# Kernel optimization log

Measured on AMD Instinct MI355X. Metric: run time of the kernel, lower is better.

Reference implementation:

```python
import jax, jax.numpy as jnp
import numpy as np

DIM = 768
NUM_HEADS = 12
HEAD_DIM = DIM // NUM_HEADS
SCALE = HEAD_DIM ** -0.5


def setup_inputs() -> dict:
    key = jax.random.key(0)
    k1, k2, k3, k4 = jax.random.split(key, 4)
    B, N, C = 4, 2048, DIM
    x = jax.random.normal(k1, (B, N, C), dtype=jnp.float32)
    # nn.Linear(dim, 3*dim, bias=False): weight shape (3C, C), y = x @ W^T
    w_qkv = jax.random.normal(k2, (3 * C, C), dtype=jnp.float32) * (C ** -0.5)
    # nn.Linear(dim, dim) with default bias=True
    w_proj = jax.random.normal(k3, (C, C), dtype=jnp.float32) * (C ** -0.5)
    b_proj = jax.random.normal(k4, (C,), dtype=jnp.float32) * 0.02
    return {"x": x, "w_qkv": w_qkv, "w_proj": w_proj, "b_proj": b_proj}


def reference(x, w_qkv, w_proj, b_proj):
    B, N, C = x.shape
    H, D = NUM_HEADS, HEAD_DIM
    qkv = jnp.einsum('bnc,oc->bno', x, w_qkv)  # (B, N, 3C)
    qkv = qkv.reshape(B, N, 3, H, D).transpose(2, 0, 3, 1, 4)  # (3, B, H, N, D)
    q, k, v = qkv[0], qkv[1], qkv[2]
    attn = jnp.einsum('bhnd,bhmd->bhnm', q, k) * jnp.float32(SCALE)  # (B,H,N,N)
    attn = jax.nn.softmax(attn, axis=-1)
    out = jnp.einsum('bhnm,bhmd->bhnd', attn, v)  # (B,H,N,D)
    out = out.transpose(0, 2, 1, 3).reshape(B, N, C)
    out = jnp.einsum('bnc,oc->bno', out, w_proj) + b_proj
    return out
```

## Files before the change

kernel.cpp:

```cpp
#include <hip/hip_runtime.h>
#include <math.h>

#define B_ 4
#define N_ 2048
#define C_ 768
#define H_ 12
#define D_ 64
#define QKSCALE_ 0.18033688011112042f

typedef unsigned short u16;
typedef unsigned int u32;
typedef short s16x8 __attribute__((ext_vector_type(8)));
typedef float f32x4 __attribute__((ext_vector_type(4)));
typedef u32 u32x2 __attribute__((ext_vector_type(2)));

__device__ __forceinline__ u16 f2bf(float f) {
    union { float f; u32 u; } v; v.f = f;
    u32 r = (v.u + 0x7fffu + ((v.u >> 16) & 1u)) >> 16;
    return (u16)r;
}

__device__ __forceinline__ u32 pkbf(float a, float b) {
    union { float f; u32 u; } ua, ub; ua.f = a; ub.f = b;
    u32 ra = ua.u + 0x7fffu + ((ua.u >> 16) & 1u);
    u32 rb = ub.u + 0x7fffu + ((ub.u >> 16) & 1u);
    return __builtin_amdgcn_perm(rb, ra, 0x07060302u);
}

__device__ __forceinline__ void gl_lds16(const u16* g, u16* l) {
    __builtin_amdgcn_global_load_lds(
        (__attribute__((address_space(1))) void*)g,
        (__attribute__((address_space(3))) void*)l, 16, 0, 0);
}

#define NX4_  (B_ * N_ * C_ / 4)
#define NWQ4_ (3 * C_ * C_ / 4)
#define NWP4_ (C_ * C_ / 4)
__global__ __launch_bounds__(256) void cvt_all(const float4* __restrict__ x,
                                               const float4* __restrict__ wq,
                                               const float4* __restrict__ wp,
                                               ushort4* __restrict__ xb,
                                               ushort4* __restrict__ wqb,
                                               ushort4* __restrict__ wpb)
{
    const int tot = NX4_ + NWQ4_ + NWP4_;
    int i = blockIdx.x * blockDim.x + threadIdx.x;
    const int stride = gridDim.x * blockDim.x;
    for (; i < tot; i += stride) {
        const float4* s; ushort4* d; int j;
        if (i < NX4_)              { s = x;  d = xb;  j = i; }
        else if (i < NX4_ + NWQ4_) { s = wq; d = wqb; j = i - NX4_; }
        else                       { s = wp; d = wpb; j = i - NX4_ - NWQ4_; }
        float4 v = s[j];
        ushort4 o;
        o.x = f2bf(v.x); o.y = f2bf(v.y); o.z = f2bf(v.z); o.w = f2bf(v.w);
        d[j] = o;
    }
}

template<int BM, int WPEU, bool OUT_BF16, bool BIAS, bool QSCALE>
__global__ __launch_bounds__(256, WPEU) void gemm_mfma(const u16* __restrict__ A,
                                                       const u16* __restrict__ Bm,
                                                       const float* __restrict__ bias,
                                                       void* __restrict__ Cout,
                                                       int M, int N, int K)
{
    constexpr int MF = BM / 32;
    constexpr int ACALLS = BM / 64;
    constexpr int ASZ = BM * 32, BSZ = 128 * 32;
    __shared__ __align__(16) u16 As[2 * ASZ];
    __shared__ __align__(16) u16 Bs[2 * BSZ];
    const int tid  = threadIdx.x;
    const int wv   = tid >> 6;
    const int lane = tid & 63;
    const int lr   = lane & 15;
    const int lq   = lane >> 4;
    const int wm   = (wv >> 1) * (BM / 2);
    const int wn   = (wv & 1) * 64;
    const int row0 = blockIdx.y * BM, col0 = blockIdx.x * 128;

    f32x4 acc[MF][4];
    #pragma unroll
    for (int i = 0; i < MF; i++)
        #pragma unroll
        for (int j = 0; j < 4; j++) { f32x4 z = {0.f,0.f,0.f,0.f}; acc[i][j] = z; }

    const int srow   = lane >> 2;
    const int schunk = (((lane & 3) ^ ((lane >> 3) & 3)) * 8);

    const int arow_base = (BM / 4) * wv;
    const u16* gA0 = A + (size_t)(row0 + arow_base + srow) * K + schunk;
    const u16* gB0 = Bm + (size_t)(col0 + 32 * wv + srow) * K + schunk;
    const u16* gB1 = gB0 + (size_t)16 * K;
    const int aoff0 = arow_base * 32;
    const int boff0 = (32 * wv) * 32, boff1 = boff0 + 16 * 32;

    const int ppos = (lq ^ ((lr >> 1) & 3)) * 8;
    const int nIter = K / 32;

    #pragma unroll
    for (int c = 0; c < ACALLS; c++)
        gl_lds16(gA0 + (size_t)(16 * c) * K, As + aoff0 + c * 16 * 32);
    gl_lds16(gB0, Bs + boff0);
    gl_lds16(gB1, Bs + boff1);

    for (int t = 0; t < nIter; t++) {
        const int cur = t & 1;
        __syncthreads();
        if (t + 1 < nIter) {
            const int k1 = (t + 1) * 32;
            const int nb = cur ^ 1;
            #pragma unroll
            for (int c = 0; c < ACALLS; c++)
                gl_lds16(gA0 + (size_t)(16 * c) * K + k1,
                         As + nb * ASZ + aoff0 + c * 16 * 32);
            gl_lds16(gB0 + k1, Bs + nb * BSZ + boff0);
            gl_lds16(gB1 + k1, Bs + nb * BSZ + boff1);
        }
        const u16* __restrict__ Ac = As + cur * ASZ;
        const u16* __restrict__ Bc = Bs + cur * BSZ;
        s16x8 af[MF], bfr[4];
        #pragma unroll
        for (int i = 0; i < MF; i++)
            af[i] = *(const s16x8*)&Ac[(wm + 16*i + lr) * 32 + ppos];
        #pragma unroll
        for (int j = 0; j < 4; j++)
            bfr[j] = *(const s16x8*)&Bc[(wn + 16*j + lr) * 32 + ppos];
        #pragma unroll
        for (int i = 0; i < MF; i++)
            #pragma unroll
            for (int j = 0; j < 4; j++)
                acc[i][j] = __builtin_amdgcn_mfma_f32_16x16x32_bf16(af[i], bfr[j], acc[i][j], 0, 0, 0);
    }

    #pragma unroll
    for (int i = 0; i < MF; i++) {
        #pragma unroll
        for (int j = 0; j < 4; j++) {
            const int col = col0 + wn + 16*j + lr;
            float bv = BIAS ? bias[col] : 0.f;
            #pragma unroll
            for (int r = 0; r < 4; r++) {
                const int row = row0 + wm + 16*i + lq*4 + r;
                float v = acc[i][j][r] + bv;
                if (QSCALE && col < C_) v *= QKSCALE_;
                if (OUT_BF16) ((u16*)Cout)[(size_t)row * N + col] = f2bf(v);
                else          ((float*)Cout)[(size_t)row * N + col] = v;
            }
        }
    }
}

__global__ __launch_bounds__(256, 4) void attn_mfma(const u16* __restrict__ qkv,
                                                    u16* __restrict__ attout)
{
    __shared__ __align__(16) u16 Ks[64 * 64];
    __shared__ __align__(16) u16 Vt[64][72];
    __shared__ __align__(16) u16 Ps[128 * 64];

    const int tid  = threadIdx.x;
    const int wv   = tid >> 6;
    const int lane = tid & 63;
    const int lr   = lane & 15;
    const int lq   = lane >> 4;
    const int n0   = blockIdx.x * 128;
    const int bh   = blockIdx.y, b = bh / H_, h = bh % H_;
    const size_t rs = 3 * C_;

    const u16* Qg = qkv + ((size_t)b * N_ + n0) * rs + h * D_;
    const u16* Kg = qkv + ((size_t)b * N_) * rs + C_ + h * D_;
    const u16* Vg = Kg + C_;

    s16x8 qf[2][2];
    #pragma unroll
    for (int iq = 0; iq < 2; iq++)
        #pragma unroll
        for (int kk = 0; kk < 2; kk++)
            qf[iq][kk] = *(const s16x8*)(Qg + (size_t)(32*wv + 16*iq + lr) * rs + kk*32 + lq*8);

    f32x4 oacc[2][4];
    float li[2] = {0.f, 0.f};
    #pragma unroll
    for (int i = 0; i < 2; i++)
        #pragma unroll
        for (int j = 0; j < 4; j++) { f32x4 z = {0.f,0.f,0.f,0.f}; oacc[i][j] = z; }

    const int skey = tid >> 2;
    const int sc0  = (tid & 3) * 2;
    const int scA  = (sc0     ^ (skey & 7)) * 8;
    const int scB  = ((sc0+1) ^ (skey & 7)) * 8;
    const int vc = tid & 7, vp = tid >> 3;
    const int vkey0 = 2 * vp, vd0 = vc * 8;
    const int vcol0 = (vkey0 + 8 * vc) & 63;

    s16x8 kr0, kr1, vr0, vr1;
    {
        const u16* kp = Kg + (size_t)skey * rs + sc0 * 8;
        kr0 = *(const s16x8*)kp; kr1 = *(const s16x8*)(kp + 8);
        const u16* vp2 = Vg + (size_t)vkey0 * rs + vd0;
        vr0 = *(const s16x8*)vp2; vr1 = *(const s16x8*)(vp2 + rs);
    }

    for (int t = 0; t < N_ / 64; t++) {
        __syncthreads();
        *(s16x8*)&Ks[skey * 64 + scA] = kr0;
        *(s16x8*)&Ks[skey * 64 + scB] = kr1;
        #pragma unroll
        for (int u = 0; u < 8; u++) {
            u32 pk = (u32)(u16)vr0[u] | ((u32)(u16)vr1[u] << 16);
            *(u32*)&Vt[vd0 + u][vcol0] = pk;
        }
        __syncthreads();
        if (t + 1 < N_ / 64) {
            const u16* kp = Kg + (size_t)((t+1)*64 + skey) * rs + sc0 * 8;
            kr0 = *(const s16x8*)kp; kr1 = *(const s16x8*)(kp + 8);
            const u16* vp2 = Vg + (size_t)((t+1)*64 + vkey0) * rs + vd0;
            vr0 = *(const s16x8*)vp2; vr1 = *(const s16x8*)(vp2 + rs);
        }

        f32x4 st[4][2];
        #pragma unroll
        for (int jk = 0; jk < 4; jk++)
            #pragma unroll
            for (int iq = 0; iq < 2; iq++) { f32x4 z = {0.f,0.f,0.f,0.f}; st[jk][iq] = z; }
        #pragma unroll
        for (int kk = 0; kk < 2; kk++) {
            s16x8 kf[4];
            #pragma unroll
            for (int jk = 0; jk < 4; jk++)
                kf[jk] = *(const s16x8*)&Ks[(16*jk + lr) * 64 + ((4*kk + lq) ^ (lr & 7)) * 8];
            #pragma unroll
            for (int jk = 0; jk < 4; jk++) {
                st[jk][0] = __builtin_amdgcn_mfma_f32_16x16x32_bf16(kf[jk], qf[0][kk], st[jk][0], 0, 0, 0);
                st[jk][1] = __builtin_amdgcn_mfma_f32_16x16x32_bf16(kf[jk], qf[1][kk], st[jk][1], 0, 0, 0);
            }
        }

        #pragma unroll
        for (int jk = 0; jk < 4; jk++)
            #pragma unroll
            for (int iq = 0; iq < 2; iq++) {
                const float p0 = __builtin_amdgcn_exp2f(st[jk][iq][0]);
                const float p1 = __builtin_amdgcn_exp2f(st[jk][iq][1]);
                const float p2 = __builtin_amdgcn_exp2f(st[jk][iq][2]);
                const float p3 = __builtin_amdgcn_exp2f(st[jk][iq][3]);
                li[iq] += (p0 + p1) + (p2 + p3);
                u32x2 w;
                w.x = pkbf(p0, p1);
                w.y = pkbf(p2, p3);
                const int prow = 32*wv + 16*iq + lr;
                const int pch  = ((2*jk + (lq >> 1)) ^ (lr & 7)) * 8 + (lq & 1) * 4;
                *(u32x2*)&Ps[prow * 64 + pch] = w;
            }

        #pragma unroll
        for (int kk = 0; kk < 2; kk++) {
            s16x8 ap0 = *(const s16x8*)&Ps[(32*wv      + lr) * 64 + ((4*kk + lq) ^ (lr & 7)) * 8];
            s16x8 ap1 = *(const s16x8*)&Ps[(32*wv + 16 + lr) * 64 + ((4*kk + lq) ^ (lr & 7)) * 8];
            #pragma unroll
            for (int j2 = 0; j2 < 4; j2++) {
                const int pb = ((kk*4 + lq) + 2*j2 + (lr >> 3)) & 7;
                s16x8 bv = *(const s16x8*)&Vt[16*j2 + lr][pb * 8];
                oacc[0][j2] = __builtin_amdgcn_mfma_f32_16x16x32_bf16(ap0, bv, oacc[0][j2], 0, 0, 0);
                oacc[1][j2] = __builtin_amdgcn_mfma_f32_16x16x32_bf16(ap1, bv, oacc[1][j2], 0, 0, 0);
            }
        }
    }

    #pragma unroll
    for (int iq = 0; iq < 2; iq++) {
        li[iq] += __shfl_xor(li[iq], 16);
        li[iq] += __shfl_xor(li[iq], 32);
    }
    #pragma unroll
    for (int iq = 0; iq < 2; iq++) {
        #pragma unroll
        for (int r = 0; r < 4; r++) {
            const float inv = 1.f / __shfl(li[iq], 4*lq + r);
            const int row = n0 + 32*wv + 16*iq + 4*lq + r;
            #pragma unroll
            for (int j2 = 0; j2 < 4; j2++)
                attout[((size_t)(b * N_ + row)) * C_ + h * D_ + 16*j2 + lr] =
                    f2bf(oacc[iq][j2][r] * inv);
        }
    }
}

extern "C" void kernel_launch(void* const* d_in, const int* in_sizes, int n_in,
                              void* d_out, int out_size, void* d_ws, size_t ws_size,
                              hipStream_t stream) {
    const float* x      = (const float*)d_in[0];
    const float* w_qkv  = (const float*)d_in[1];
    const float* w_proj = (const float*)d_in[2];
    const float* b_proj = (const float*)d_in[3];
    float* out = (float*)d_out;

    const int NX   = B_ * N_ * C_;
    const int NWQ  = 3 * C_ * C_;
    const int NWP  = C_ * C_;
    const int NQKV = B_ * N_ * 3 * C_;

    u16* xb   = (u16*)d_ws;
    u16* wqb  = xb + NX;
    u16* wpb  = wqb + NWQ;
    u16* qkvb = wpb + NWP;
    u16* attb = qkvb + NQKV;

    dim3 blk(256);

    cvt_all<<<768, blk, 0, stream>>>((const float4*)x, (const float4*)w_qkv,
                                     (const float4*)w_proj,
                                     (ushort4*)xb, (ushort4*)wqb, (ushort4*)wpb);

    const int M = B_ * N_;
    gemm_mfma<256, 2, true, false, true><<<dim3((3*C_)/128, M/256), blk, 0, stream>>>(
        xb, wqb, nullptr, qkvb, M, 3*C_, C_);

    attn_mfma<<<dim3(N_/128, B_ * H_), blk, 0, stream>>>(qkvb, attb);

    gemm_mfma<64, 4, false, true, false><<<dim3(C_/128, M/64), blk, 0, stream>>>(
        attb, wpb, b_proj, out, M, C_, C_);
}
```

Measured before the change: 241.8 us.

## Deepen GEMM K-tile to 64 and double-buffer K/V tiles in attention

The GEMM kernel now stages a K-slice of 64 instead of 32 per iteration, using a wider XOR swizzle and two MFMA sub-steps per tile, which halves the number of barriers and loop iterations. The QKV GEMM drops from BM=256 to BM=128 to produce more blocks, and occupancy hints are lowered to fit the larger LDS footprint. The attention kernel double-buffers the K and V^T shared tiles and prefetches two tiles ahead, removing one __syncthreads per iteration. The cost is more LDS per block and lower occupancy.

```diff
diff --git a/kernel.cpp b/kernel.cpp
--- a/kernel.cpp
+++ b/kernel.cpp
@@ -65,9 +65,9 @@
                                                        void* __restrict__ Cout,
                                                        int M, int N, int K)
 {
-    constexpr int MF = BM / 32;
-    constexpr int ACALLS = BM / 64;
-    constexpr int ASZ = BM * 32, BSZ = 128 * 32;
+    constexpr int MF  = BM / 32;
+    constexpr int AC  = BM / 32;
+    constexpr int ASZ = BM * 64, BSZ = 128 * 64;
     __shared__ __align__(16) u16 As[2 * ASZ];
     __shared__ __align__(16) u16 Bs[2 * BSZ];
     const int tid  = threadIdx.x;
@@ -85,52 +85,55 @@
         #pragma unroll
         for (int j = 0; j < 4; j++) { f32x4 z = {0.f,0.f,0.f,0.f}; acc[i][j] = z; }
 
-    const int srow   = lane >> 2;
-    const int schunk = (((lane & 3) ^ ((lane >> 3) & 3)) * 8);
+    const int srow   = lane >> 3;
+    const int schunk = ((lane & 7) ^ srow) * 8;
 
     const int arow_base = (BM / 4) * wv;
-    const u16* gA0 = A + (size_t)(row0 + arow_base + srow) * K + schunk;
-    const u16* gB0 = Bm + (size_t)(col0 + 32 * wv + srow) * K + schunk;
-    const u16* gB1 = gB0 + (size_t)16 * K;
-    const int aoff0 = arow_base * 32;
-    const int boff0 = (32 * wv) * 32, boff1 = boff0 + 16 * 32;
-
-    const int ppos = (lq ^ ((lr >> 1) & 3)) * 8;
-    const int nIter = K / 32;
-
-    #pragma unroll
-    for (int c = 0; c < ACALLS; c++)
-        gl_lds16(gA0 + (size_t)(16 * c) * K, As + aoff0 + c * 16 * 32);
-    gl_lds16(gB0, Bs + boff0);
-    gl_lds16(gB1, Bs + boff1);
+    const u16* gA = A + (size_t)(row0 + arow_base + srow) * K + schunk;
+    const u16* gB = Bm + (size_t)(col0 + 32 * wv + srow) * K + schunk;
+    const int aoff = arow_base * 64;
+    const int boff = (32 * wv) * 64;
+
+    const int nIter = K / 64;
+
+    #pragma unroll
+    for (int c = 0; c < AC; c++)
+        gl_lds16(gA + (size_t)(8 * c) * K, As + aoff + c * 8 * 64);
+    #pragma unroll
+    for (int c = 0; c < 4; c++)
+        gl_lds16(gB + (size_t)(8 * c) * K, Bs + boff + c * 8 * 64);
 
     for (int t = 0; t < nIter; t++) {
         const int cur = t & 1;
         __syncthreads();
         if (t + 1 < nIter) {
-            const int k1 = (t + 1) * 32;
+            const int k1 = (t + 1) * 64;
             const int nb = cur ^ 1;
             #pragma unroll
-            for (int c = 0; c < ACALLS; c++)
-                gl_lds16(gA0 + (size_t)(16 * c) * K + k1,
-                         As + nb * ASZ + aoff0 + c * 16 * 32);
-            gl_lds16(gB0 + k1, Bs + nb * BSZ + boff0);
-            gl_lds16(gB1 + k1, Bs + nb * BSZ + boff1);
+            for (int c = 0; c < AC; c++)
+                gl_lds16(gA + (size_t)(8 * c) * K + k1, As + nb * ASZ + aoff + c * 8 * 64);
+            #pragma unroll
+            for (int c = 0; c < 4; c++)
+                gl_lds16(gB + (size_t)(8 * c) * K + k1, Bs + nb * BSZ + boff + c * 8 * 64);
         }
         const u16* __restrict__ Ac = As + cur * ASZ;
         const u16* __restrict__ Bc = Bs + cur * BSZ;
-        s16x8 af[MF], bfr[4];
-        #pragma unroll
-        for (int i = 0; i < MF; i++)
-            af[i] = *(const s16x8*)&Ac[(wm + 16*i + lr) * 32 + ppos];
-        #pragma unroll
-        for (int j = 0; j < 4; j++)
-            bfr[j] = *(const s16x8*)&Bc[(wn + 16*j + lr) * 32 + ppos];
-        #pragma unroll
-        for (int i = 0; i < MF; i++)
+        #pragma unroll
+        for (int kk = 0; kk < 2; kk++) {
+            const int fo = ((4 * kk + lq) ^ (lr & 7)) * 8;
+            s16x8 af[MF], bfr[4];
+            #pragma unroll
+            for (int i = 0; i < MF; i++)
+                af[i] = *(const s16x8*)&Ac[(wm + 16*i + lr) * 64 + fo];
             #pragma unroll
             for (int j = 0; j < 4; j++)
-                acc[i][j] = __builtin_amdgcn_mfma_f32_16x16x32_bf16(af[i], bfr[j], acc[i][j], 0, 0, 0);
+                bfr[j] = *(const s16x8*)&Bc[(wn + 16*j + lr) * 64 + fo];
+            #pragma unroll
+            for (int i = 0; i < MF; i++)
+                #pragma unroll
+                for (int j = 0; j < 4; j++)
+                    acc[i][j] = __builtin_amdgcn_mfma_f32_16x16x32_bf16(af[i], bfr[j], acc[i][j], 0, 0, 0);
+        }
     }
 
     #pragma unroll
@@ -151,11 +154,11 @@
     }
 }
 
-__global__ __launch_bounds__(256, 4) void attn_mfma(const u16* __restrict__ qkv,
+__global__ __launch_bounds__(256, 3) void attn_mfma(const u16* __restrict__ qkv,
                                                     u16* __restrict__ attout)
 {
-    __shared__ __align__(16) u16 Ks[64 * 64];
-    __shared__ __align__(16) u16 Vt[64][72];
+    __shared__ __align__(16) u16 Ks[2][64 * 64];
+    __shared__ __align__(16) u16 Vt[2][64][72];
     __shared__ __align__(16) u16 Ps[128 * 64];
 
     const int tid  = threadIdx.x;
@@ -200,21 +203,37 @@
         const u16* vp2 = Vg + (size_t)vkey0 * rs + vd0;
         vr0 = *(const s16x8*)vp2; vr1 = *(const s16x8*)(vp2 + rs);
     }
-
-    for (int t = 0; t < N_ / 64; t++) {
+    *(s16x8*)&Ks[0][skey * 64 + scA] = kr0;
+    *(s16x8*)&Ks[0][skey * 64 + scB] = kr1;
+    #pragma unroll
+    for (int u = 0; u < 8; u++) {
+        u32 pk = (u32)(u16)vr0[u] | ((u32)(u16)vr1[u] << 16);
+        *(u32*)&Vt[0][vd0 + u][vcol0] = pk;
+    }
+    {
+        const u16* kp = Kg + (size_t)(64 + skey) * rs + sc0 * 8;
+        kr0 = *(const s16x8*)kp; kr1 = *(const s16x8*)(kp + 8);
+        const u16* vp2 = Vg + (size_t)(64 + vkey0) * rs + vd0;
+        vr0 = *(const s16x8*)vp2; vr1 = *(const s16x8*)(vp2 + rs);
+    }
+
+    const int NT = N_ / 64;
+    for (int t = 0; t < NT; t++) {
+        const int cur = t & 1, nxt = cur ^ 1;
         __syncthreads();
-        *(s16x8*)&Ks[skey * 64 + scA] = kr0;
-        *(s16x8*)&Ks[skey * 64 + scB] = kr1;
-        #pragma unroll
-        for (int u = 0; u < 8; u++) {
-            u32 pk = (u32)(u16)vr0[u] | ((u32)(u16)vr1[u] << 16);
-            *(u32*)&Vt[vd0 + u][vcol0] = pk;
-        }
-        __syncthreads();
-        if (t + 1 < N_ / 64) {
-            const u16* kp = Kg + (size_t)((t+1)*64 + skey) * rs + sc0 * 8;
+        if (t + 1 < NT) {
+            *(s16x8*)&Ks[nxt][skey * 64 + scA] = kr0;
+            *(s16x8*)&Ks[nxt][skey * 64 + scB] = kr1;
+            #pragma unroll
+            for (int u = 0; u < 8; u++) {
+                u32 pk = (u32)(u16)vr0[u] | ((u32)(u16)vr1[u] << 16);
+                *(u32*)&Vt[nxt][vd0 + u][vcol0] = pk;
+            }
+        }
+        if (t + 2 < NT) {
+            const u16* kp = Kg + (size_t)((t+2)*64 + skey) * rs + sc0 * 8;
             kr0 = *(const s16x8*)kp; kr1 = *(const s16x8*)(kp + 8);
-            const u16* vp2 = Vg + (size_t)((t+1)*64 + vkey0) * rs + vd0;
+            const u16* vp2 = Vg + (size_t)((t+2)*64 + vkey0) * rs + vd0;
             vr0 = *(const s16x8*)vp2; vr1 = *(const s16x8*)(vp2 + rs);
         }
 
@@ -228,7 +247,7 @@
             s16x8 kf[4];
             #pragma unroll
             for (int jk = 0; jk < 4; jk++)
-                kf[jk] = *(const s16x8*)&Ks[(16*jk + lr) * 64 + ((4*kk + lq) ^ (lr & 7)) * 8];
+                kf[jk] = *(const s16x8*)&Ks[cur][(16*jk + lr) * 64 + ((4*kk + lq) ^ (lr & 7)) * 8];
             #pragma unroll
             for (int jk = 0; jk < 4; jk++) {
                 st[jk][0] = __builtin_amdgcn_mfma_f32_16x16x32_bf16(kf[jk], qf[0][kk], st[jk][0], 0, 0, 0);
@@ -260,7 +279,7 @@
             #pragma unroll
             for (int j2 = 0; j2 < 4; j2++) {
                 const int pb = ((kk*4 + lq) + 2*j2 + (lr >> 3)) & 7;
-                s16x8 bv = *(const s16x8*)&Vt[16*j2 + lr][pb * 8];
+                s16x8 bv = *(const s16x8*)&Vt[cur][16*j2 + lr][pb * 8];
                 oacc[0][j2] = __builtin_amdgcn_mfma_f32_16x16x32_bf16(ap0, bv, oacc[0][j2], 0, 0, 0);
                 oacc[1][j2] = __builtin_amdgcn_mfma_f32_16x16x32_bf16(ap1, bv, oacc[1][j2], 0, 0, 0);
             }
@@ -313,11 +332,11 @@
                                      (ushort4*)xb, (ushort4*)wqb, (ushort4*)wpb);
 
     const int M = B_ * N_;
-    gemm_mfma<256, 2, true, false, true><<<dim3((3*C_)/128, M/256), blk, 0, stream>>>(
+    gemm_mfma<128, 2, true, false, true><<<dim3((3*C_)/128, M/128), blk, 0, stream>>>(
         xb, wqb, nullptr, qkvb, M, 3*C_, C_);
 
     attn_mfma<<<dim3(N_/128, B_ * H_), blk, 0, stream>>>(qkvb, attb);
 
-    gemm_mfma<64, 4, false, true, false><<<dim3(C_/128, M/64), blk, 0, stream>>>(
+    gemm_mfma<64, 3, false, true, false><<<dim3(C_/128, M/64), blk, 0, stream>>>(
         attb, wpb, b_proj, out, M, C_, C_);
 }
```

Result: faster. 218.7 us (-9.6%).
